# Kernel optimization log

Hardware: AMD Instinct MI355X
Metric: run time of the kernel (lower is better)

## Reference

```python
import jax, jax.numpy as jnp
import numpy as np

B, S, C = 4, 2048, 1024
E, H = 1024, 16
D = E // H  # head_dim = 64


def setup_inputs() -> dict:
    key = jax.random.key(0)
    k1, k2, k3, k4, k5 = jax.random.split(key, 5)
    s = 1.0 / np.sqrt(C)
    return {
        "x": jax.random.normal(k1, (B, S, C), dtype=jnp.float32),
        "w_qkv": jax.random.uniform(k2, (C, 3 * E), minval=-s, maxval=s, dtype=jnp.float32),
        "b_qkv": jax.random.uniform(k3, (3 * E,), minval=-s, maxval=s, dtype=jnp.float32),
        "w_out": jax.random.uniform(k4, (E, E), minval=-1.0 / np.sqrt(E), maxval=1.0 / np.sqrt(E), dtype=jnp.float32),
        "b_out": jax.random.uniform(k5, (E,), minval=-1.0 / np.sqrt(E), maxval=1.0 / np.sqrt(E), dtype=jnp.float32),
    }


def reference(x, w_qkv, b_qkv, w_out, b_out):
    b, s, _ = x.shape
    qkv = x @ w_qkv + b_qkv                      # [B,S,3E]
    qkv = qkv.reshape(b, s, 3, H, D)
    q = qkv[:, :, 0].transpose(0, 2, 1, 3)       # [B,H,S,D]
    k = qkv[:, :, 1].transpose(0, 2, 1, 3)
    v = qkv[:, :, 2].transpose(0, 2, 1, 3)
    scale = jnp.asarray(D, x.dtype) ** 0.5
    scores = jnp.einsum("bhqd,bhkd->bhqk", q, k) / scale
    attn = jax.nn.softmax(scores, axis=-1)       # dropout is identity in eval mode
    out = jnp.einsum("bhqk,bhkd->bhqd", attn, v)
    out = out.transpose(0, 2, 1, 3).reshape(b, s, E)
    return out @ w_out + b_out
```

## Files before the change

kernel.cpp:

```cpp
#include <hip/hip_runtime.h>


typedef _Float16 f16;
typedef f16 f16x2 __attribute__((ext_vector_type(2)));
typedef f16 f16x4 __attribute__((ext_vector_type(4)));
typedef f16 f16x8 __attribute__((ext_vector_type(8)));
typedef float f32x4 __attribute__((ext_vector_type(4)));

typedef const __attribute__((address_space(1))) void* gas_ptr;
typedef __attribute__((address_space(3))) void* lds_ptr;

__device__ __forceinline__ void load_lds16(const void* g, void* s) {
  __builtin_amdgcn_global_load_lds((gas_ptr)g, (lds_ptr)s, 16, 0, 0);
}

__device__ __forceinline__ f32x4 mfma16(f16x8 a, f16x8 b, f32x4 c) {
  return __builtin_amdgcn_mfma_f32_16x16x32_f16(a, b, c, 0, 0, 0);
}

__device__ __forceinline__ f16x2 pk2(float a, float b) {
  return __builtin_bit_cast(f16x2, __builtin_amdgcn_cvt_pkrtz(a, b));
}

__global__ __launch_bounds__(256) void cvt_x(const float* __restrict__ in, f16* __restrict__ out) {
  int i = blockIdx.x * 256 + threadIdx.x;
  const float4* p = (const float4*)in;
  float4 a = p[2 * i], b = p[2 * i + 1];
  f16x8 o;
  o[0] = (f16)a.x; o[1] = (f16)a.y; o[2] = (f16)a.z; o[3] = (f16)a.w;
  o[4] = (f16)b.x; o[5] = (f16)b.y; o[6] = (f16)b.z; o[7] = (f16)b.w;
  *(f16x8*)(out + 8 * (long)i) = o;
}

__global__ __launch_bounds__(256) void tconv(const float* __restrict__ in, f16* __restrict__ out,
                                             int R, int C) {
  __shared__ float t[32][33];
  int c0 = blockIdx.x * 32, r0 = blockIdx.y * 32;
  int tx = threadIdx.x, ty = threadIdx.y;
#pragma unroll
  for (int j = 0; j < 4; ++j)
    t[ty + 8 * j][tx] = in[(long)(r0 + ty + 8 * j) * C + c0 + tx];
  __syncthreads();
#pragma unroll
  for (int j = 0; j < 4; ++j)
    out[(long)(c0 + ty + 8 * j) * R + r0 + tx] = (f16)t[tx][ty + 8 * j];
}

__global__ __launch_bounds__(256) void qkv_gemm(const f16* __restrict__ A, const f16* __restrict__ BT,
                                                const float* __restrict__ bias,
                                                f16* __restrict__ Qs, f16* __restrict__ Kk,
                                                f16* __restrict__ Vt) {
  __shared__ __align__(16) f16 lA[128 * 64];
  __shared__ __align__(16) f16 lB[128 * 64];
  const int K = 1024;
  int tid = threadIdx.x, w = tid >> 6, lane = tid & 63, l16 = lane & 15, quad = lane >> 4;
  int wm = (w >> 1) * 64, wn = (w & 1) * 64;
  int id = blockIdx.y * gridDim.x + blockIdx.x;
  int xcd = id & 7, cch = id >> 3;
  int bx = xcd * 8 + (cch & 7), by = cch >> 3;
  int blockM = bx * 128, blockN = by * 128;
  int sw = l16 & 7;
  f32x4 acc[4][4] = {};

  for (int k0 = 0; k0 < K; k0 += 64) {
    __syncthreads();
#pragma unroll
    for (int i = 0; i < 4; ++i) {
      int c = i * 256 + tid;
      int row = c >> 3;
      int sc = (c & 7) ^ (row & 7);
      load_lds16(A + (blockM + row) * K + k0 + sc * 8, lA + c * 8);
      load_lds16(BT + (blockN + row) * K + k0 + sc * 8, lB + c * 8);
    }
    __syncthreads();
#pragma unroll
    for (int ks = 0; ks < 2; ++ks) {
      f16x8 af[4], bf[4];
#pragma unroll
      for (int mb = 0; mb < 4; ++mb)
        af[mb] = *(const f16x8*)&lA[(wm + mb * 16 + l16) * 64 + ((ks * 4 + quad) ^ sw) * 8];
#pragma unroll
      for (int nb = 0; nb < 4; ++nb)
        bf[nb] = *(const f16x8*)&lB[(wn + nb * 16 + l16) * 64 + ((ks * 4 + quad) ^ sw) * 8];
#pragma unroll
      for (int mb = 0; mb < 4; ++mb)
#pragma unroll
        for (int nb = 0; nb < 4; ++nb)
          acc[mb][nb] = mfma16(af[mb], bf[nb], acc[mb][nb]);
    }
  }

  int which = by >> 3;
  const float SCALE = 0.18033688011112042f;
#pragma unroll
  for (int nb = 0; nb < 4; ++nb) {
    int col = blockN + wn + nb * 16 + l16;
    int hd = col & 1023, h = hd >> 6, d = hd & 63;
    float bv = bias[col];
#pragma unroll
    for (int mb = 0; mb < 4; ++mb) {
      int row0 = blockM + wm + mb * 16 + quad * 4;
      int b = row0 >> 11, s0 = row0 & 2047;
      if (which == 2) {
        f16x2 a = pk2(acc[mb][nb][0] + bv, acc[mb][nb][1] + bv);
        f16x2 c = pk2(acc[mb][nb][2] + bv, acc[mb][nb][3] + bv);
        *(f16x4*)&Vt[((b * 16 + h) * 64 + d) * 2048 + s0] =
            __builtin_shufflevector(a, c, 0, 1, 2, 3);
      } else if (which == 0) {
#pragma unroll
        for (int r = 0; r < 4; ++r)
          Qs[((b * 16 + h) * 2048 + s0 + r) * 64 + d] = (f16)((acc[mb][nb][r] + bv) * SCALE);
      } else {
#pragma unroll
        for (int r = 0; r < 4; ++r)
          Kk[((b * 16 + h) * 2048 + s0 + r) * 64 + d] = (f16)(acc[mb][nb][r] + bv);
      }
    }
  }
}

__global__ __launch_bounds__(512, 4) void attn(const f16* __restrict__ Qs, const f16* __restrict__ Kk,
                                               const f16* __restrict__ Vt, f16* __restrict__ ctx) {
  __shared__ __align__(16) f16 lK[2][64 * 72];
  __shared__ __align__(16) f16 lV[2][64 * 72];
  int id = blockIdx.y * gridDim.x + blockIdx.x;
  int swz = (id & 7) * 64 + (id >> 3);
  int qt = swz & 7, bh = swz >> 3;
  int tid = threadIdx.x, lane = tid & 63, l16 = lane & 15, quad = lane >> 4;
  int w = tid >> 6;
  const f16* Qbase = Qs + ((long)bh * 2048 + qt * 256 + w * 32) * 64;
  const f16* Kbh = Kk + (long)bh * 2048 * 64;
  const f16* Vbh = Vt + (long)bh * 64 * 2048;

  f16x8 qf[2][2];
#pragma unroll
  for (int rb = 0; rb < 2; ++rb)
#pragma unroll
    for (int ks = 0; ks < 2; ++ks)
      qf[rb][ks] = *(const f16x8*)(Qbase + (rb * 16 + l16) * 64 + ks * 32 + quad * 8);

  f32x4 of[2][4] = {};
  f32x4 osum[2] = {};
  const f16 one = (f16)1.f;
  const f16x8 vone8 = {one, one, one, one, one, one, one, one};

  int rs = tid >> 3, o = (tid & 7) * 8;
  int koff = o & 31;
  int cperm = (o & 32) + ((koff & 12) << 1) + ((koff >> 4) << 2);

  {
    *(float4*)&lK[0][rs * 72 + o] = *(const float4*)(Kbh + rs * 64 + o);
    float4 pv = *(const float4*)(Vbh + (long)rs * 2048 + o);
    f16x8 v8 = __builtin_bit_cast(f16x8, pv);
    *(f16x4*)&lV[0][rs * 72 + cperm] = __builtin_shufflevector(v8, v8, 0, 1, 2, 3);
    *(f16x4*)&lV[0][rs * 72 + cperm + 8] = __builtin_shufflevector(v8, v8, 4, 5, 6, 7);
  }
  __syncthreads();

  for (int kt = 0; kt < 32; ++kt) {
    int cur = kt & 1, nxt = cur ^ 1;

    float4 pk0, pv0;
    if (kt < 31) {
      int kb0 = (kt + 1) * 64;
      pk0 = *(const float4*)(Kbh + (kb0 + rs) * 64 + o);
      pv0 = *(const float4*)(Vbh + (long)rs * 2048 + kb0 + o);
    }

    __builtin_amdgcn_s_setprio(1);
#pragma unroll
    for (int kp = 0; kp < 2; ++kp) {
      f16x4 pah[2][2];
#pragma unroll
      for (int kbh = 0; kbh < 2; ++kbh) {
        int kb = kp * 2 + kbh;
        f16x8 kf0 = *(const f16x8*)&lK[cur][(kb * 16 + l16) * 72 + quad * 8];
        f16x8 kf1 = *(const f16x8*)&lK[cur][(kb * 16 + l16) * 72 + 32 + quad * 8];
#pragma unroll
        for (int rb = 0; rb < 2; ++rb) {
          f32x4 z = {};
          z = mfma16(kf0, qf[rb][0], z);
          z = mfma16(kf1, qf[rb][1], z);
          float p0 = __builtin_amdgcn_exp2f(z[0]);
          float p1 = __builtin_amdgcn_exp2f(z[1]);
          float p2 = __builtin_amdgcn_exp2f(z[2]);
          float p3 = __builtin_amdgcn_exp2f(z[3]);
          pah[rb][kbh] = __builtin_shufflevector(pk2(p0, p1), pk2(p2, p3), 0, 1, 2, 3);
        }
      }
      f16x8 pa[2];
      pa[0] = __builtin_shufflevector(pah[0][0], pah[0][1], 0, 1, 2, 3, 4, 5, 6, 7);
      pa[1] = __builtin_shufflevector(pah[1][0], pah[1][1], 0, 1, 2, 3, 4, 5, 6, 7);

#pragma unroll
      for (int db = 0; db < 4; ++db) {
        f16x8 vf = *(const f16x8*)&lV[cur][(db * 16 + l16) * 72 + kp * 32 + quad * 8];
#pragma unroll
        for (int rb = 0; rb < 2; ++rb)
          of[rb][db] = mfma16(pa[rb], vf, of[rb][db]);
      }
#pragma unroll
      for (int rb = 0; rb < 2; ++rb)
        osum[rb] = mfma16(pa[rb], vone8, osum[rb]);
    }
    __builtin_amdgcn_s_setprio(0);

    if (kt < 31) {
      *(float4*)&lK[nxt][rs * 72 + o] = pk0;
      f16x8 v8 = __builtin_bit_cast(f16x8, pv0);
      *(f16x4*)&lV[nxt][rs * 72 + cperm] = __builtin_shufflevector(v8, v8, 0, 1, 2, 3);
      *(f16x4*)&lV[nxt][rs * 72 + cperm + 8] = __builtin_shufflevector(v8, v8, 4, 5, 6, 7);
      __syncthreads();
    }
  }

  int b = bh >> 4, h = bh & 15;
  long token0 = (long)b * 2048 + qt * 256 + w * 32;
#pragma unroll
  for (int rb = 0; rb < 2; ++rb) {
    float inv[4];
#pragma unroll
    for (int r = 0; r < 4; ++r) inv[r] = 1.0f / osum[rb][r];
#pragma unroll
    for (int db = 0; db < 4; ++db)
#pragma unroll
      for (int r = 0; r < 4; ++r)
        ctx[(token0 + rb * 16 + quad * 4 + r) * 1024 + h * 64 + db * 16 + l16] =
            (f16)(of[rb][db][r] * inv[r]);
  }
}

__global__ __launch_bounds__(256) void proj_gemm(const f16* __restrict__ A, const f16* __restrict__ BT,
                                                 const float* __restrict__ bias,
                                                 float* __restrict__ out) {
  __shared__ __align__(16) f16 lA[128 * 64];
  __shared__ __align__(16) f16 lB[128 * 64];
  const int K = 1024;
  int tid = threadIdx.x, w = tid >> 6, lane = tid & 63, l16 = lane & 15, quad = lane >> 4;
  int wm = (w >> 1) * 64, wn = (w & 1) * 64;
  int id = blockIdx.y * gridDim.x + blockIdx.x;
  int xcd = id & 7, cch = id >> 3;
  int bx = xcd * 8 + (cch & 7), by = cch >> 3;
  int blockM = bx * 128, blockN = by * 128;
  int sw = l16 & 7;
  f32x4 acc[4][4] = {};

  for (int k0 = 0; k0 < K; k0 += 64) {
    __syncthreads();
#pragma unroll
    for (int i = 0; i < 4; ++i) {
      int c = i * 256 + tid;
      int row = c >> 3;
      int sc = (c & 7) ^ (row & 7);
      load_lds16(A + (blockM + row) * K + k0 + sc * 8, lA + c * 8);
      load_lds16(BT + (blockN + row) * K + k0 + sc * 8, lB + c * 8);
    }
    __syncthreads();
#pragma unroll
    for (int ks = 0; ks < 2; ++ks) {
      f16x8 af[4], bf[4];
#pragma unroll
      for (int mb = 0; mb < 4; ++mb)
        af[mb] = *(const f16x8*)&lA[(wm + mb * 16 + l16) * 64 + ((ks * 4 + quad) ^ sw) * 8];
#pragma unroll
      for (int nb = 0; nb < 4; ++nb)
        bf[nb] = *(const f16x8*)&lB[(wn + nb * 16 + l16) * 64 + ((ks * 4 + quad) ^ sw) * 8];
#pragma unroll
      for (int mb = 0; mb < 4; ++mb)
#pragma unroll
        for (int nb = 0; nb < 4; ++nb)
          acc[mb][nb] = mfma16(af[mb], bf[nb], acc[mb][nb]);
    }
  }

#pragma unroll
  for (int nb = 0; nb < 4; ++nb) {
    int col = blockN + wn + nb * 16 + l16;
    float bv = bias[col];
#pragma unroll
    for (int mb = 0; mb < 4; ++mb) {
#pragma unroll
      for (int r = 0; r < 4; ++r) {
        int row = blockM + wm + mb * 16 + quad * 4 + r;
        out[(long)row * 1024 + col] = acc[mb][nb][r] + bv;
      }
    }
  }
}

extern "C" void kernel_launch(void* const* d_in, const int* in_sizes, int n_in,
                              void* d_out, int out_size, void* d_ws, size_t ws_size,
                              hipStream_t stream) {
  const float* x     = (const float*)d_in[0];
  const float* w_qkv = (const float*)d_in[1];
  const float* b_qkv = (const float*)d_in[2];
  const float* w_out = (const float*)d_in[3];
  const float* b_out = (const float*)d_in[4];
  float* out = (float*)d_out;

  char* ws = (char*)d_ws;
  f16* xh    = (f16*)(ws);
  f16* ctx   = (f16*)(ws);
  f16* wqkvT = (f16*)(ws + 16777216);
  f16* woutT = (f16*)(ws + 23068672);
  f16* Qs    = (f16*)(ws + 25165824);
  f16* Kk    = (f16*)(ws + 41943040);
  f16* Vt    = (f16*)(ws + 58720256);

  cvt_x<<<4096, 256, 0, stream>>>(x, xh);
  tconv<<<dim3(96, 32), dim3(32, 8), 0, stream>>>(w_qkv, wqkvT, 1024, 3072);
  tconv<<<dim3(32, 32), dim3(32, 8), 0, stream>>>(w_out, woutT, 1024, 1024);
  qkv_gemm<<<dim3(64, 24), 256, 0, stream>>>(xh, wqkvT, b_qkv, Qs, Kk, Vt);
  attn<<<dim3(8, 64), 512, 0, stream>>>(Qs, Kk, Vt, ctx);
  proj_gemm<<<dim3(64, 8), 256, 0, stream>>>(ctx, woutT, b_out, out);
}
```

Baseline: 267.1 us.

## Restructure QKV GEMM into 256x256 tiles with double-buffered async LDS pipeline

The QKV projection GEMM moves from 128x128 tiles with 4 waves to 256x256 tiles with 8 waves. Each wave now computes a 128x64 sub-tile. K-tiles are double-buffered in LDS, and the global-to-LDS loads for the next tiles are interleaved between MFMA phases using explicit vmcnt waits, barriers and setprio. The aim is to hide memory latency behind compute and raise arithmetic intensity per loaded byte. In exchange it uses 128KB of LDS per block, produces far fewer blocks (384), and relies on a delicate manual synchronisation schedule.

```diff
diff --git a/kernel.cpp b/kernel.cpp
--- a/kernel.cpp
+++ b/kernel.cpp
@@ -46,74 +46,115 @@
     out[(long)(c0 + ty + 8 * j) * R + r0 + tx] = (f16)t[tx][ty + 8 * j];
 }
 
-__global__ __launch_bounds__(256) void qkv_gemm(const f16* __restrict__ A, const f16* __restrict__ BT,
-                                                const float* __restrict__ bias,
-                                                f16* __restrict__ Qs, f16* __restrict__ Kk,
-                                                f16* __restrict__ Vt) {
-  __shared__ __align__(16) f16 lA[128 * 64];
-  __shared__ __align__(16) f16 lB[128 * 64];
+__global__ __launch_bounds__(512, 2) void qkv_gemm(const f16* __restrict__ A, const f16* __restrict__ BT,
+                                                   const float* __restrict__ bias,
+                                                   f16* __restrict__ Qs, f16* __restrict__ Kk,
+                                                   f16* __restrict__ Vt) {
+  __shared__ __align__(16) f16 lA[2][256 * 64];
+  __shared__ __align__(16) f16 lB[2][256 * 64];
   const int K = 1024;
   int tid = threadIdx.x, w = tid >> 6, lane = tid & 63, l16 = lane & 15, quad = lane >> 4;
-  int wm = (w >> 1) * 64, wn = (w & 1) * 64;
+  int wr = w >> 2, wc = w & 3;
   int id = blockIdx.y * gridDim.x + blockIdx.x;
   int xcd = id & 7, cch = id >> 3;
-  int bx = xcd * 8 + (cch & 7), by = cch >> 3;
-  int blockM = bx * 128, blockN = by * 128;
+  int bx = xcd * 4 + (cch & 3), by = cch >> 2;
+  int blockM = bx * 256, blockN = by * 256;
   int sw = l16 & 7;
-  f32x4 acc[4][4] = {};
-
-  for (int k0 = 0; k0 < K; k0 += 64) {
-    __syncthreads();
-#pragma unroll
-    for (int i = 0; i < 4; ++i) {
-      int c = i * 256 + tid;
-      int row = c >> 3;
-      int sc = (c & 7) ^ (row & 7);
-      load_lds16(A + (blockM + row) * K + k0 + sc * 8, lA + c * 8);
-      load_lds16(BT + (blockN + row) * K + k0 + sc * 8, lB + c * 8);
-    }
-    __syncthreads();
-#pragma unroll
-    for (int ks = 0; ks < 2; ++ks) {
-      f16x8 af[4], bf[4];
-#pragma unroll
-      for (int mb = 0; mb < 4; ++mb)
-        af[mb] = *(const f16x8*)&lA[(wm + mb * 16 + l16) * 64 + ((ks * 4 + quad) ^ sw) * 8];
-#pragma unroll
-      for (int nb = 0; nb < 4; ++nb)
-        bf[nb] = *(const f16x8*)&lB[(wn + nb * 16 + l16) * 64 + ((ks * 4 + quad) ^ sw) * 8];
-#pragma unroll
-      for (int mb = 0; mb < 4; ++mb)
-#pragma unroll
-        for (int nb = 0; nb < 4; ++nb)
-          acc[mb][nb] = mfma16(af[mb], bf[nb], acc[mb][nb]);
-    }
-  }
-
-  int which = by >> 3;
+  f32x4 acc[8][4] = {};
+
+  auto stA = [&](int kt, int h) {
+    f16* dst = lA[kt & 1];
+    int k0 = (kt & 15) << 6;
+#pragma unroll
+    for (int j = 0; j < 2; ++j) {
+      int br = j * 128 + h * 64 + w * 8;
+      int r = br + (lane >> 3);
+      int sc = (lane & 7) ^ (r & 7);
+      load_lds16(A + (long)(blockM + r) * K + k0 + sc * 8, dst + br * 64);
+    }
+  };
+  auto stB = [&](int kt, int h) {
+    f16* dst = lB[kt & 1];
+    int k0 = (kt & 15) << 6;
+#pragma unroll
+    for (int j = 0; j < 2; ++j) {
+      int br = j * 128 + (w >> 2) * 64 + h * 32 + (w & 3) * 8;
+      int r = br + (lane >> 3);
+      int sc = (lane & 7) ^ (r & 7);
+      load_lds16(BT + (long)(blockN + r) * K + k0 + sc * 8, dst + br * 64);
+    }
+  };
+
+  stA(0, 0); stA(0, 1); stB(0, 0); stB(0, 1);
+  stA(1, 0); stB(1, 0);
+  asm volatile("s_waitcnt vmcnt(4)" ::: "memory");
+  __builtin_amdgcn_s_barrier();
+
+  for (int t = 0; t < 16; ++t) {
+    const f16* cA = lA[t & 1];
+    const f16* cB = lB[t & 1];
+#pragma unroll
+    for (int p = 0; p < 4; ++p) {
+      const int mh = p >> 1, nh = p & 1;
+      f16x8 af[4][2], bf[2][2];
+#pragma unroll
+      for (int mf = 0; mf < 4; ++mf) {
+        int rowA = wr * 128 + (mh * 4 + mf) * 16 + l16;
+#pragma unroll
+        for (int kk = 0; kk < 2; ++kk)
+          af[mf][kk] = *(const f16x8*)&cA[rowA * 64 + ((kk * 4 + quad) ^ sw) * 8];
+      }
+#pragma unroll
+      for (int nf = 0; nf < 2; ++nf) {
+        int rowB = wc * 64 + (nh * 2 + nf) * 16 + l16;
+#pragma unroll
+        for (int kk = 0; kk < 2; ++kk)
+          bf[nf][kk] = *(const f16x8*)&cB[rowB * 64 + ((kk * 4 + quad) ^ sw) * 8];
+      }
+      if (p == 0) stA(t + 1, 1);
+      else if (p == 1) stB(t + 1, 1);
+      else if (p == 2) stA(t + 2, 0);
+      else stB(t + 2, 0);
+      __builtin_amdgcn_s_barrier();
+      __builtin_amdgcn_s_setprio(1);
+#pragma unroll
+      for (int mf = 0; mf < 4; ++mf)
+#pragma unroll
+        for (int nf = 0; nf < 2; ++nf)
+#pragma unroll
+          for (int kk = 0; kk < 2; ++kk)
+            acc[mh * 4 + mf][nh * 2 + nf] =
+                mfma16(af[mf][kk], bf[nf][kk], acc[mh * 4 + mf][nh * 2 + nf]);
+      __builtin_amdgcn_s_setprio(0);
+      if (p == 3) asm volatile("s_waitcnt vmcnt(4)" ::: "memory");
+      __builtin_amdgcn_s_barrier();
+    }
+  }
+
+  int which = by >> 2;
   const float SCALE = 0.18033688011112042f;
 #pragma unroll
-  for (int nb = 0; nb < 4; ++nb) {
-    int col = blockN + wn + nb * 16 + l16;
+  for (int nf = 0; nf < 4; ++nf) {
+    int col = blockN + wc * 64 + nf * 16 + l16;
     int hd = col & 1023, h = hd >> 6, d = hd & 63;
     float bv = bias[col];
 #pragma unroll
-    for (int mb = 0; mb < 4; ++mb) {
-      int row0 = blockM + wm + mb * 16 + quad * 4;
+    for (int mf = 0; mf < 8; ++mf) {
+      int row0 = blockM + wr * 128 + mf * 16 + quad * 4;
       int b = row0 >> 11, s0 = row0 & 2047;
       if (which == 2) {
-        f16x2 a = pk2(acc[mb][nb][0] + bv, acc[mb][nb][1] + bv);
-        f16x2 c = pk2(acc[mb][nb][2] + bv, acc[mb][nb][3] + bv);
+        f16x2 a = pk2(acc[mf][nf][0] + bv, acc[mf][nf][1] + bv);
+        f16x2 c = pk2(acc[mf][nf][2] + bv, acc[mf][nf][3] + bv);
         *(f16x4*)&Vt[((b * 16 + h) * 64 + d) * 2048 + s0] =
             __builtin_shufflevector(a, c, 0, 1, 2, 3);
       } else if (which == 0) {
 #pragma unroll
         for (int r = 0; r < 4; ++r)
-          Qs[((b * 16 + h) * 2048 + s0 + r) * 64 + d] = (f16)((acc[mb][nb][r] + bv) * SCALE);
+          Qs[((b * 16 + h) * 2048 + s0 + r) * 64 + d] = (f16)((acc[mf][nf][r] + bv) * SCALE);
       } else {
 #pragma unroll
         for (int r = 0; r < 4; ++r)
-          Kk[((b * 16 + h) * 2048 + s0 + r) * 64 + d] = (f16)(acc[mb][nb][r] + bv);
+          Kk[((b * 16 + h) * 2048 + s0 + r) * 64 + d] = (f16)(acc[mf][nf][r] + bv);
       }
     }
   }
@@ -310,7 +351,7 @@
   cvt_x<<<4096, 256, 0, stream>>>(x, xh);
   tconv<<<dim3(96, 32), dim3(32, 8), 0, stream>>>(w_qkv, wqkvT, 1024, 3072);
   tconv<<<dim3(32, 32), dim3(32, 8), 0, stream>>>(w_out, woutT, 1024, 1024);
-  qkv_gemm<<<dim3(64, 24), 256, 0, stream>>>(xh, wqkvT, b_qkv, Qs, Kk, Vt);
+  qkv_gemm<<<dim3(32, 12), 512, 0, stream>>>(xh, wqkvT, b_qkv, Qs, Kk, Vt);
   attn<<<dim3(8, 64), 512, 0, stream>>>(Qs, Kk, Vt, ctx);
   proj_gemm<<<dim3(64, 8), 256, 0, stream>>>(ctx, woutT, b_out, out);
 }
```

Result: slower. 279.1 us (+4.5%).

## Double-buffer LDS tiles in QKV and projection GEMMs to overlap loads with MFMA

Applied to the files above, without the earlier changes.

Both GEMM kernels now hold two LDS buffers per operand and prefetch the next K tile with global_load_lds while MFMAs run on the current one. This leaves a single vmcnt wait and barrier per iteration instead of two barriers around a blocking load. It also raises wave priority around the MFMA block. LDS use doubles to 64KB per block, which may lower occupancy. The LDS reads before the barrier are assumed to be waited on by the compiler-inserted lgkmcnt before the next iteration overwrites that buffer.

```diff
diff --git a/kernel.cpp b/kernel.cpp
--- a/kernel.cpp
+++ b/kernel.cpp
@@ -50,8 +50,8 @@
                                                 const float* __restrict__ bias,
                                                 f16* __restrict__ Qs, f16* __restrict__ Kk,
                                                 f16* __restrict__ Vt) {
-  __shared__ __align__(16) f16 lA[128 * 64];
-  __shared__ __align__(16) f16 lB[128 * 64];
+  __shared__ __align__(16) f16 lA[2][128 * 64];
+  __shared__ __align__(16) f16 lB[2][128 * 64];
   const int K = 1024;
   int tid = threadIdx.x, w = tid >> 6, lane = tid & 63, l16 = lane & 15, quad = lane >> 4;
   int wm = (w >> 1) * 64, wn = (w & 1) * 64;
@@ -62,32 +62,47 @@
   int sw = l16 & 7;
   f32x4 acc[4][4] = {};
 
-  for (int k0 = 0; k0 < K; k0 += 64) {
-    __syncthreads();
+  auto stage = [&](int kt) {
+    int k0 = kt * 64;
+    f16* dA = lA[kt & 1];
+    f16* dB = lB[kt & 1];
 #pragma unroll
     for (int i = 0; i < 4; ++i) {
       int c = i * 256 + tid;
       int row = c >> 3;
       int sc = (c & 7) ^ (row & 7);
-      load_lds16(A + (blockM + row) * K + k0 + sc * 8, lA + c * 8);
-      load_lds16(BT + (blockN + row) * K + k0 + sc * 8, lB + c * 8);
-    }
-    __syncthreads();
+      load_lds16(A + (long)(blockM + row) * K + k0 + sc * 8, dA + c * 8);
+      load_lds16(BT + (long)(blockN + row) * K + k0 + sc * 8, dB + c * 8);
+    }
+  };
+
+  stage(0);
+  asm volatile("s_waitcnt vmcnt(0)" ::: "memory");
+  __builtin_amdgcn_s_barrier();
+
+  for (int t = 0; t < 16; ++t) {
+    if (t < 15) stage(t + 1);
+    const f16* cA = lA[t & 1];
+    const f16* cB = lB[t & 1];
 #pragma unroll
     for (int ks = 0; ks < 2; ++ks) {
       f16x8 af[4], bf[4];
 #pragma unroll
       for (int mb = 0; mb < 4; ++mb)
-        af[mb] = *(const f16x8*)&lA[(wm + mb * 16 + l16) * 64 + ((ks * 4 + quad) ^ sw) * 8];
+        af[mb] = *(const f16x8*)&cA[(wm + mb * 16 + l16) * 64 + ((ks * 4 + quad) ^ sw) * 8];
 #pragma unroll
       for (int nb = 0; nb < 4; ++nb)
-        bf[nb] = *(const f16x8*)&lB[(wn + nb * 16 + l16) * 64 + ((ks * 4 + quad) ^ sw) * 8];
+        bf[nb] = *(const f16x8*)&cB[(wn + nb * 16 + l16) * 64 + ((ks * 4 + quad) ^ sw) * 8];
+      __builtin_amdgcn_s_setprio(1);
 #pragma unroll
       for (int mb = 0; mb < 4; ++mb)
 #pragma unroll
         for (int nb = 0; nb < 4; ++nb)
           acc[mb][nb] = mfma16(af[mb], bf[nb], acc[mb][nb]);
-    }
+      __builtin_amdgcn_s_setprio(0);
+    }
+    asm volatile("s_waitcnt vmcnt(0)" ::: "memory");
+    __builtin_amdgcn_s_barrier();
   }
 
   int which = by >> 3;
@@ -233,8 +248,8 @@
 __global__ __launch_bounds__(256) void proj_gemm(const f16* __restrict__ A, const f16* __restrict__ BT,
                                                  const float* __restrict__ bias,
                                                  float* __restrict__ out) {
-  __shared__ __align__(16) f16 lA[128 * 64];
-  __shared__ __align__(16) f16 lB[128 * 64];
+  __shared__ __align__(16) f16 lA[2][128 * 64];
+  __shared__ __align__(16) f16 lB[2][128 * 64];
   const int K = 1024;
   int tid = threadIdx.x, w = tid >> 6, lane = tid & 63, l16 = lane & 15, quad = lane >> 4;
   int wm = (w >> 1) * 64, wn = (w & 1) * 64;
@@ -245,32 +260,47 @@
   int sw = l16 & 7;
   f32x4 acc[4][4] = {};
 
-  for (int k0 = 0; k0 < K; k0 += 64) {
-    __syncthreads();
+  auto stage = [&](int kt) {
+    int k0 = kt * 64;
+    f16* dA = lA[kt & 1];
+    f16* dB = lB[kt & 1];
 #pragma unroll
     for (int i = 0; i < 4; ++i) {
       int c = i * 256 + tid;
       int row = c >> 3;
       int sc = (c & 7) ^ (row & 7);
-      load_lds16(A + (blockM + row) * K + k0 + sc * 8, lA + c * 8);
-      load_lds16(BT + (blockN + row) * K + k0 + sc * 8, lB + c * 8);
-    }
-    __syncthreads();
+      load_lds16(A + (long)(blockM + row) * K + k0 + sc * 8, dA + c * 8);
+      load_lds16(BT + (long)(blockN + row) * K + k0 + sc * 8, dB + c * 8);
+    }
+  };
+
+  stage(0);
+  asm volatile("s_waitcnt vmcnt(0)" ::: "memory");
+  __builtin_amdgcn_s_barrier();
+
+  for (int t = 0; t < 16; ++t) {
+    if (t < 15) stage(t + 1);
+    const f16* cA = lA[t & 1];
+    const f16* cB = lB[t & 1];
 #pragma unroll
     for (int ks = 0; ks < 2; ++ks) {
       f16x8 af[4], bf[4];
 #pragma unroll
       for (int mb = 0; mb < 4; ++mb)
-        af[mb] = *(const f16x8*)&lA[(wm + mb * 16 + l16) * 64 + ((ks * 4 + quad) ^ sw) * 8];
+        af[mb] = *(const f16x8*)&cA[(wm + mb * 16 + l16) * 64 + ((ks * 4 + quad) ^ sw) * 8];
 #pragma unroll
       for (int nb = 0; nb < 4; ++nb)
-        bf[nb] = *(const f16x8*)&lB[(wn + nb * 16 + l16) * 64 + ((ks * 4 + quad) ^ sw) * 8];
+        bf[nb] = *(const f16x8*)&cB[(wn + nb * 16 + l16) * 64 + ((ks * 4 + quad) ^ sw) * 8];
+      __builtin_amdgcn_s_setprio(1);
 #pragma unroll
       for (int mb = 0; mb < 4; ++mb)
 #pragma unroll
         for (int nb = 0; nb < 4; ++nb)
           acc[mb][nb] = mfma16(af[mb], bf[nb], acc[mb][nb]);
-    }
+      __builtin_amdgcn_s_setprio(0);
+    }
+    asm volatile("s_waitcnt vmcnt(0)" ::: "memory");
+    __builtin_amdgcn_s_barrier();
   }
 
 #pragma unroll
```

Result: faster. 257.8 us (-3.5%).
